# Performance work log

Hardware: AMD Instinct MI355X
Metric: run time of the kernel (lower is better)

## Reference

```python
import jax, jax.numpy as jnp
import numpy as np

B, L = 64, 1024
ENC_DIM, DEC_DIM, ATT_DIM = 512, 512, 512


def setup_inputs() -> dict:
    key = jax.random.key(0)
    ks = jax.random.split(key, 11)
    s_enc = 1.0 / np.sqrt(ENC_DIM)
    s_dec = 1.0 / np.sqrt(DEC_DIM)
    s_att = 1.0 / np.sqrt(ATT_DIM)
    return {
        "encoder_features": jax.random.normal(ks[0], (B, L, ENC_DIM), jnp.float32),
        "decoder_hidden": jax.random.normal(ks[1], (B, DEC_DIM), jnp.float32),
        "coverage": jax.random.uniform(ks[2], (B, L), jnp.float32),
        # nn.Linear params (torch stores weight as [out, in]; we keep [in, out])
        "W_enc": jax.random.uniform(ks[3], (ENC_DIM, ATT_DIM), jnp.float32, -s_enc, s_enc),
        "b_enc": jax.random.uniform(ks[4], (ATT_DIM,), jnp.float32, -s_enc, s_enc),
        "W_dec": jax.random.uniform(ks[5], (DEC_DIM, ATT_DIM), jnp.float32, -s_dec, s_dec),
        "b_dec": jax.random.uniform(ks[6], (ATT_DIM,), jnp.float32, -s_dec, s_dec),
        "W_cov": jax.random.uniform(ks[7], (1, ATT_DIM), jnp.float32, -1.0, 1.0),
        "b_cov": jax.random.uniform(ks[8], (ATT_DIM,), jnp.float32, -1.0, 1.0),
        "W_full": jax.random.uniform(ks[9], (ATT_DIM, 1), jnp.float32, -s_att, s_att),
        "b_full": jax.random.uniform(ks[10], (1,), jnp.float32, -s_att, s_att),
    }


def reference(encoder_features, decoder_hidden, coverage,
              W_enc, b_enc, W_dec, b_dec, W_cov, b_cov, W_full, b_full):
    # att1: [B, L, A]
    att1 = jnp.einsum("ble,ea->bla", encoder_features, W_enc) + b_enc
    # att2: [B, 1, A]
    att2 = (decoder_hidden @ W_dec + b_dec)[:, None, :]
    # att3: coverage[B,L] through Linear(1, A) -> outer product, [B, L, A]
    att3 = coverage[:, :, None] * W_cov[0] + b_cov
    # energy: [B, L]
    energy = (jax.nn.relu(att1 + att2 + att3) @ W_full)[:, :, 0] + b_full[0]
    alpha = jax.nn.softmax(energy, axis=1)  # [B, L]
    new_coverage = coverage + alpha
    attention_weighted_encoding = jnp.einsum("ble,bl->be", encoder_features, alpha)
    return (attention_weighted_encoding, alpha, new_coverage)
```

## Files before the change

### kernel.cpp

```cpp
#include <hip/hip_runtime.h>
#include <cstdint>
#include <cstddef>

#define NB   64
#define NL   1024
#define NA   512
#define NE   512
#define NROWS (NB*NL)

typedef __attribute__((ext_vector_type(8))) short bf16x8;
typedef __attribute__((ext_vector_type(4))) float f32x4;

__device__ __forceinline__ unsigned short f2bf(float x){
    unsigned int u = __float_as_uint(x);
    u += 0x7FFFu + ((u >> 16) & 1u);
    return (unsigned short)(u >> 16);
}

__global__ __launch_bounds__(256) void k_wfrag(const float* __restrict__ Wenc,
                                               unsigned short* __restrict__ wfrag){
    const int g    = blockIdx.x * 256 + threadIdx.x;
    const int lane = g & 63;
    const int n    = (g >> 6) & 31;
    const int ks   = (g >> 11) & 1;
    const int s    = g >> 12;
    const int col  = n * 16 + (lane & 15);
    const int kb   = s * 64 + ks * 32 + (lane >> 4) * 8;
    unsigned int w[4];
    #pragma unroll
    for (int p = 0; p < 4; ++p){
        unsigned short lo = f2bf(Wenc[(size_t)(kb + 2*p    ) * NA + col]);
        unsigned short hi = f2bf(Wenc[(size_t)(kb + 2*p + 1) * NA + col]);
        w[p] = (unsigned int)lo | ((unsigned int)hi << 16);
    }
    ((uint4*)wfrag)[g] = make_uint4(w[0], w[1], w[2], w[3]);
}

__global__ __launch_bounds__(256) void k_base(const float* __restrict__ dh,
                                              const float* __restrict__ Wdec,
                                              const float* __restrict__ bdec,
                                              const float* __restrict__ benc,
                                              const float* __restrict__ bcov,
                                              float* __restrict__ base){
    const int b   = blockIdx.x >> 3;
    const int a0  = (blockIdx.x & 7) * 64;
    const int tid = threadIdx.x;
    const int al  = tid & 63, kg = tid >> 6;
    __shared__ float h[512];
    __shared__ float ps[4][64];
    h[tid]       = dh[b * 512 + tid];
    h[tid + 256] = dh[b * 512 + tid + 256];
    __syncthreads();
    const float* wp = Wdec + (size_t)(kg * 128) * 512 + a0 + al;
    const float* hp = h + kg * 128;
    float s0 = 0.f, s1 = 0.f, s2 = 0.f, s3 = 0.f;
    #pragma unroll
    for (int k = 0; k < 128; k += 4){
        s0 += hp[k + 0] * wp[(size_t)(k + 0) * 512];
        s1 += hp[k + 1] * wp[(size_t)(k + 1) * 512];
        s2 += hp[k + 2] * wp[(size_t)(k + 2) * 512];
        s3 += hp[k + 3] * wp[(size_t)(k + 3) * 512];
    }
    ps[kg][al] = (s0 + s1) + (s2 + s3);
    __syncthreads();
    if (tid < 64){
        const int a = a0 + tid;
        base[b * 512 + a] = ps[0][tid] + ps[1][tid] + ps[2][tid] + ps[3][tid]
                          + bdec[a] + benc[a] + bcov[a];
    }
}

__global__ __launch_bounds__(256, 2) void k_energy(
        const float* __restrict__ enc,
        const float* __restrict__ cov,
        const float* __restrict__ base,
        const unsigned short* __restrict__ wfrag,
        const float* __restrict__ Wcov,
        const float* __restrict__ Wfull,
        float* __restrict__ energy)
{
    __shared__ __align__(16) unsigned char sB[65536];
    __shared__ __align__(16) unsigned char sA[8192];
    __shared__ float sCov[64];
    __shared__ float sEp[4][64];

    const int tid  = threadIdx.x;
    const int wid  = tid >> 6, lane = tid & 63;
    const int r0   = blockIdx.x * 64;
    const int b    = r0 >> 10;

    if (tid < 64) sCov[tid] = cov[r0 + tid];

    f32x4 acc[4][8];
    #pragma unroll
    for (int m = 0; m < 4; ++m)
        #pragma unroll
        for (int n = 0; n < 8; ++n) acc[m][n] = (f32x4){0.f, 0.f, 0.f, 0.f};

    const int rloc = tid >> 2, q = tid & 3;
    const float* arow = enc + (size_t)(r0 + rloc) * NE + q * 16;
    unsigned char* aw = sA + (((q >> 1) * 4 + (rloc >> 4)) * 1024
                              + ((rloc & 15) + 32 * (q & 1)) * 16);
    const unsigned char* bsrc = (const unsigned char*)wfrag + wid * 16384 + lane * 16;
    unsigned char* bdst = sB + wid * 16384;

    for (int s = 0; s < 8; ++s){
        __syncthreads();
        const unsigned char* bs = bsrc + (size_t)s * 65536;
        #pragma unroll
        for (int i = 0; i < 16; ++i){
            __builtin_amdgcn_global_load_lds(
                (__attribute__((address_space(1))) void*)(bs + i * 1024),
                (__attribute__((address_space(3))) void*)(bdst + i * 1024),
                16, 0, 0);
        }
        const float* ap = arow + s * 64;
        float4 v0 = *(const float4*)(ap);
        float4 v1 = *(const float4*)(ap + 4);
        float4 v2 = *(const float4*)(ap + 8);
        float4 v3 = *(const float4*)(ap + 12);
        uint4 f1, f2;
        f1.x = f2bf(v0.x) | ((unsigned)f2bf(v0.y) << 16);
        f1.y = f2bf(v0.z) | ((unsigned)f2bf(v0.w) << 16);
        f1.z = f2bf(v1.x) | ((unsigned)f2bf(v1.y) << 16);
        f1.w = f2bf(v1.z) | ((unsigned)f2bf(v1.w) << 16);
        f2.x = f2bf(v2.x) | ((unsigned)f2bf(v2.y) << 16);
        f2.y = f2bf(v2.z) | ((unsigned)f2bf(v2.w) << 16);
        f2.z = f2bf(v3.x) | ((unsigned)f2bf(v3.y) << 16);
        f2.w = f2bf(v3.z) | ((unsigned)f2bf(v3.w) << 16);
        *(uint4*)(aw)       = f1;
        *(uint4*)(aw + 256) = f2;
        __syncthreads();
        bf16x8 af[2][4];
        #pragma unroll
        for (int ks = 0; ks < 2; ++ks)
            #pragma unroll
            for (int m = 0; m < 4; ++m)
                af[ks][m] = *(const bf16x8*)(sA + (ks*4 + m) * 1024 + lane * 16);
        #pragma unroll
        for (int ks = 0; ks < 2; ++ks){
            #pragma unroll
            for (int n = 0; n < 8; ++n){
                bf16x8 bfr = *(const bf16x8*)(sB + (ks*32 + wid*8 + n) * 1024 + lane * 16);
                #pragma unroll
                for (int m = 0; m < 4; ++m)
                    acc[m][n] = __builtin_amdgcn_mfma_f32_16x16x32_bf16(
                                    af[ks][m], bfr, acc[m][n], 0, 0, 0);
            }
        }
    }

    const int c0 = wid * 128 + (lane & 15);
    float basev[8], wcovv[8], wfullv[8];
    #pragma unroll
    for (int n = 0; n < 8; ++n){
        const int c = c0 + n * 16;
        basev[n]  = base[b * 512 + c];
        wcovv[n]  = Wcov[c];
        wfullv[n] = Wfull[c];
    }
    const int hi = lane >> 4;
    float covr[4][4];
    #pragma unroll
    for (int m = 0; m < 4; ++m)
        #pragma unroll
        for (int r = 0; r < 4; ++r) covr[m][r] = sCov[m*16 + 4*hi + r];
    float epv[4][4] = {};
    #pragma unroll
    for (int m = 0; m < 4; ++m)
        #pragma unroll
        for (int n = 0; n < 8; ++n)
            #pragma unroll
            for (int r = 0; r < 4; ++r){
                float v = acc[m][n][r] + basev[n] + covr[m][r] * wcovv[n];
                v = fmaxf(v, 0.f);
                epv[m][r] += v * wfullv[n];
            }
    #pragma unroll
    for (int m = 0; m < 4; ++m)
        #pragma unroll
        for (int r = 0; r < 4; ++r){
            float v = epv[m][r];
            v += __shfl_xor(v, 1);
            v += __shfl_xor(v, 2);
            v += __shfl_xor(v, 4);
            v += __shfl_xor(v, 8);
            epv[m][r] = v;
        }
    if ((lane & 15) == 0){
        #pragma unroll
        for (int m = 0; m < 4; ++m)
            #pragma unroll
            for (int r = 0; r < 4; ++r)
                sEp[wid][m*16 + 4*hi + r] = epv[m][r];
    }
    __syncthreads();
    if (tid < 64)
        energy[r0 + tid] = sEp[0][tid] + sEp[1][tid] + sEp[2][tid] + sEp[3][tid];
}

#define AWE_OFF   0
#define ALPHA_OFF 32768
#define NCOV_OFF  98304

__global__ __launch_bounds__(256) void k_finish(
        const float* __restrict__ enc, const float* __restrict__ cov,
        const float* __restrict__ energy, float* __restrict__ out)
{
    const int bid = blockIdx.x;
    const int b = bid >> 3, ec = bid & 7;
    const int tid = threadIdx.x;
    __shared__ float sa[1024];
    __shared__ float rb[16];
    __shared__ float ps[4][64];

    float4 ev = ((const float4*)(energy + b * 1024))[tid];
    float mx = fmaxf(fmaxf(ev.x, ev.y), fmaxf(ev.z, ev.w));
    #pragma unroll
    for (int off = 32; off; off >>= 1) mx = fmaxf(mx, __shfl_xor(mx, off));
    if ((tid & 63) == 0) rb[tid >> 6] = mx;
    __syncthreads();
    mx = fmaxf(fmaxf(rb[0], rb[1]), fmaxf(rb[2], rb[3]));
    float e0 = __expf(ev.x - mx), e1 = __expf(ev.y - mx),
          e2 = __expf(ev.z - mx), e3 = __expf(ev.w - mx);
    ((float4*)sa)[tid] = make_float4(e0, e1, e2, e3);
    float sm = e0 + e1 + e2 + e3;
    #pragma unroll
    for (int off = 32; off; off >>= 1) sm += __shfl_xor(sm, off);
    if ((tid & 63) == 0) rb[8 + (tid >> 6)] = sm;
    __syncthreads();
    const float inv = 1.0f / (rb[8] + rb[9] + rb[10] + rb[11]);

    if (ec == 0){
        #pragma unroll
        for (int i = 0; i < 4; ++i){
            const int idx = tid + i * 256;
            const float a = sa[idx] * inv;
            out[ALPHA_OFF + b * 1024 + idx] = a;
            out[NCOV_OFF  + b * 1024 + idx] = cov[b * 1024 + idx] + a;
        }
    }

    const int qt = tid >> 6, cl = tid & 63;
    const float* ep = enc + ((size_t)(b * 1024 + qt * 256)) * 512 + ec * 64 + cl;
    const float* w = sa + qt * 256;
    float a0 = 0.f, a1 = 0.f, a2 = 0.f, a3 = 0.f;
    for (int l = 0; l < 256; l += 4){
        a0 += ep[(size_t)(l + 0) * 512] * w[l + 0];
        a1 += ep[(size_t)(l + 1) * 512] * w[l + 1];
        a2 += ep[(size_t)(l + 2) * 512] * w[l + 2];
        a3 += ep[(size_t)(l + 3) * 512] * w[l + 3];
    }
    ps[qt][cl] = (a0 + a1) + (a2 + a3);
    __syncthreads();
    if (tid < 64)
        out[AWE_OFF + b * 512 + ec * 64 + tid] =
            (ps[0][tid] + ps[1][tid] + ps[2][tid] + ps[3][tid]) * inv;
}

extern "C" void kernel_launch(void* const* d_in, const int* in_sizes, int n_in,
                              void* d_out, int out_size, void* d_ws, size_t ws_size,
                              hipStream_t stream){
    const float* enc   = (const float*)d_in[0];
    const float* dh    = (const float*)d_in[1];
    const float* cov   = (const float*)d_in[2];
    const float* Wenc  = (const float*)d_in[3];
    const float* benc  = (const float*)d_in[4];
    const float* Wdec  = (const float*)d_in[5];
    const float* bdec  = (const float*)d_in[6];
    const float* Wcov  = (const float*)d_in[7];
    const float* bcov  = (const float*)d_in[8];
    const float* Wfull = (const float*)d_in[9];
    float* out = (float*)d_out;

    unsigned short* wfrag = (unsigned short*)d_ws;
    float* base   = (float*)((char*)d_ws + 512 * 1024);
    float* energy = (float*)((char*)d_ws + 640 * 1024);

    k_wfrag <<<128,  256, 0, stream>>>(Wenc, wfrag);
    k_base  <<<512,  256, 0, stream>>>(dh, Wdec, bdec, benc, bcov, base);
    k_energy<<<1024, 256, 0, stream>>>(enc, cov, base, wfrag, Wcov, Wfull, energy);
    k_finish<<<512,  256, 0, stream>>>(enc, cov, energy, out);
}
```

Before: 85.16 us.

## Restructure energy GEMM: 128-row tiles, B fragments in registers, double-buffered A

The energy kernel now processes 128 rows per block with 8 waves, each wave owning 64 output columns. The W_enc fragments are loaded straight from global memory into registers instead of staging the whole 64 KB B tile in LDS. The A tile is double-buffered in LDS so the next k-slice's loads and bf16 conversion overlap the current MFMAs, with one barrier per step. The weight fragment layout is reordered to match. This cuts LDS use and traffic and improves overlap, at the cost of higher register pressure from register-resident B (current and next) with 512-thread blocks.

```diff
diff --git a/kernel.cpp b/kernel.cpp
--- a/kernel.cpp
+++ b/kernel.cpp
@@ -6,7 +6,6 @@
 #define NL   1024
 #define NA   512
 #define NE   512
-#define NROWS (NB*NL)
 
 typedef __attribute__((ext_vector_type(8))) short bf16x8;
 typedef __attribute__((ext_vector_type(4))) float f32x4;
@@ -21,10 +20,11 @@
                                                unsigned short* __restrict__ wfrag){
     const int g    = blockIdx.x * 256 + threadIdx.x;
     const int lane = g & 63;
-    const int n    = (g >> 6) & 31;
-    const int ks   = (g >> 11) & 1;
+    const int n    = (g >> 6) & 3;
+    const int ks   = (g >> 8) & 1;
+    const int cw   = (g >> 9) & 7;
     const int s    = g >> 12;
-    const int col  = n * 16 + (lane & 15);
+    const int col  = cw * 64 + n * 16 + (lane & 15);
     const int kb   = s * 64 + ks * 32 + (lane >> 4) * 8;
     unsigned int w[4];
     #pragma unroll
@@ -70,7 +70,7 @@
     }
 }
 
-__global__ __launch_bounds__(256, 2) void k_energy(
+__global__ __launch_bounds__(512, 2) void k_energy(
         const float* __restrict__ enc,
         const float* __restrict__ cov,
         const float* __restrict__ base,
@@ -79,46 +79,38 @@
         const float* __restrict__ Wfull,
         float* __restrict__ energy)
 {
-    __shared__ __align__(16) unsigned char sB[65536];
-    __shared__ __align__(16) unsigned char sA[8192];
-    __shared__ float sCov[64];
-    __shared__ float sEp[4][64];
+    __shared__ __align__(16) unsigned char sA[2][16384];
+    __shared__ float sEp[8][128];
+    __shared__ float sCov[128];
 
     const int tid  = threadIdx.x;
     const int wid  = tid >> 6, lane = tid & 63;
-    const int r0   = blockIdx.x * 64;
+    const int r0   = blockIdx.x * 128;
     const int b    = r0 >> 10;
 
-    if (tid < 64) sCov[tid] = cov[r0 + tid];
-
-    f32x4 acc[4][8];
-    #pragma unroll
-    for (int m = 0; m < 4; ++m)
-        #pragma unroll
-        for (int n = 0; n < 8; ++n) acc[m][n] = (f32x4){0.f, 0.f, 0.f, 0.f};
+    if (tid < 128) sCov[tid] = cov[r0 + tid];
 
     const int rloc = tid >> 2, q = tid & 3;
     const float* arow = enc + (size_t)(r0 + rloc) * NE + q * 16;
-    unsigned char* aw = sA + (((q >> 1) * 4 + (rloc >> 4)) * 1024
-                              + ((rloc & 15) + 32 * (q & 1)) * 16);
-    const unsigned char* bsrc = (const unsigned char*)wfrag + wid * 16384 + lane * 16;
-    unsigned char* bdst = sB + wid * 16384;
-
-    for (int s = 0; s < 8; ++s){
-        __syncthreads();
-        const unsigned char* bs = bsrc + (size_t)s * 65536;
-        #pragma unroll
-        for (int i = 0; i < 16; ++i){
-            __builtin_amdgcn_global_load_lds(
-                (__attribute__((address_space(1))) void*)(bs + i * 1024),
-                (__attribute__((address_space(3))) void*)(bdst + i * 1024),
-                16, 0, 0);
-        }
-        const float* ap = arow + s * 64;
-        float4 v0 = *(const float4*)(ap);
-        float4 v1 = *(const float4*)(ap + 4);
-        float4 v2 = *(const float4*)(ap + 8);
-        float4 v3 = *(const float4*)(ap + 12);
+    const int awoff = ((q >> 1) * 8 + (rloc >> 4)) * 1024
+                    + ((rloc & 15) + 32 * (q & 1)) * 16;
+
+    const bf16x8* bbase = (const bf16x8*)wfrag + wid * 512 + lane;
+
+    f32x4 acc[8][4];
+    #pragma unroll
+    for (int m = 0; m < 8; ++m)
+        #pragma unroll
+        for (int n = 0; n < 4; ++n) acc[m][n] = (f32x4){0.f, 0.f, 0.f, 0.f};
+
+    bf16x8 bcur[8], bnxt[8];
+    #pragma unroll
+    for (int j = 0; j < 8; ++j) bcur[j] = bbase[j * 64];
+    {
+        float4 v0 = *(const float4*)(arow);
+        float4 v1 = *(const float4*)(arow + 4);
+        float4 v2 = *(const float4*)(arow + 8);
+        float4 v3 = *(const float4*)(arow + 12);
         uint4 f1, f2;
         f1.x = f2bf(v0.x) | ((unsigned)f2bf(v0.y) << 16);
         f1.y = f2bf(v0.z) | ((unsigned)f2bf(v0.w) << 16);
@@ -128,56 +120,84 @@
         f2.y = f2bf(v2.z) | ((unsigned)f2bf(v2.w) << 16);
         f2.z = f2bf(v3.x) | ((unsigned)f2bf(v3.y) << 16);
         f2.w = f2bf(v3.z) | ((unsigned)f2bf(v3.w) << 16);
-        *(uint4*)(aw)       = f1;
-        *(uint4*)(aw + 256) = f2;
+        *(uint4*)(sA[0] + awoff)       = f1;
+        *(uint4*)(sA[0] + awoff + 256) = f2;
+    }
+    __syncthreads();
+
+    #pragma unroll
+    for (int s = 0; s < 8; ++s){
+        const int cb = s & 1;
+        float4 av0, av1, av2, av3;
+        if (s < 7){
+            const float* ap = arow + (s + 1) * 64;
+            av0 = *(const float4*)(ap);
+            av1 = *(const float4*)(ap + 4);
+            av2 = *(const float4*)(ap + 8);
+            av3 = *(const float4*)(ap + 12);
+            const bf16x8* bp = bbase + (s + 1) * 4096;
+            #pragma unroll
+            for (int j = 0; j < 8; ++j) bnxt[j] = bp[j * 64];
+        }
+        #pragma unroll
+        for (int ks = 0; ks < 2; ++ks){
+            bf16x8 af[8];
+            #pragma unroll
+            for (int m = 0; m < 8; ++m)
+                af[m] = *(const bf16x8*)(sA[cb] + (ks * 8 + m) * 1024 + lane * 16);
+            #pragma unroll
+            for (int n = 0; n < 4; ++n)
+                #pragma unroll
+                for (int m = 0; m < 8; ++m)
+                    acc[m][n] = __builtin_amdgcn_mfma_f32_16x16x32_bf16(
+                                    af[m], bcur[ks * 4 + n], acc[m][n], 0, 0, 0);
+        }
+        if (s < 7){
+            uint4 f1, f2;
+            f1.x = f2bf(av0.x) | ((unsigned)f2bf(av0.y) << 16);
+            f1.y = f2bf(av0.z) | ((unsigned)f2bf(av0.w) << 16);
+            f1.z = f2bf(av1.x) | ((unsigned)f2bf(av1.y) << 16);
+            f1.w = f2bf(av1.z) | ((unsigned)f2bf(av1.w) << 16);
+            f2.x = f2bf(av2.x) | ((unsigned)f2bf(av2.y) << 16);
+            f2.y = f2bf(av2.z) | ((unsigned)f2bf(av2.w) << 16);
+            f2.z = f2bf(av3.x) | ((unsigned)f2bf(av3.y) << 16);
+            f2.w = f2bf(av3.z) | ((unsigned)f2bf(av3.w) << 16);
+            *(uint4*)(sA[cb ^ 1] + awoff)       = f1;
+            *(uint4*)(sA[cb ^ 1] + awoff + 256) = f2;
+            #pragma unroll
+            for (int j = 0; j < 8; ++j) bcur[j] = bnxt[j];
+        }
         __syncthreads();
-        bf16x8 af[2][4];
-        #pragma unroll
-        for (int ks = 0; ks < 2; ++ks)
-            #pragma unroll
-            for (int m = 0; m < 4; ++m)
-                af[ks][m] = *(const bf16x8*)(sA + (ks*4 + m) * 1024 + lane * 16);
-        #pragma unroll
-        for (int ks = 0; ks < 2; ++ks){
-            #pragma unroll
-            for (int n = 0; n < 8; ++n){
-                bf16x8 bfr = *(const bf16x8*)(sB + (ks*32 + wid*8 + n) * 1024 + lane * 16);
-                #pragma unroll
-                for (int m = 0; m < 4; ++m)
-                    acc[m][n] = __builtin_amdgcn_mfma_f32_16x16x32_bf16(
-                                    af[ks][m], bfr, acc[m][n], 0, 0, 0);
-            }
-        }
-    }
-
-    const int c0 = wid * 128 + (lane & 15);
-    float basev[8], wcovv[8], wfullv[8];
-    #pragma unroll
-    for (int n = 0; n < 8; ++n){
+    }
+
+    const int c0 = wid * 64 + (lane & 15);
+    float basev[4], wcovv[4], wfullv[4];
+    #pragma unroll
+    for (int n = 0; n < 4; ++n){
         const int c = c0 + n * 16;
         basev[n]  = base[b * 512 + c];
         wcovv[n]  = Wcov[c];
         wfullv[n] = Wfull[c];
     }
     const int hi = lane >> 4;
-    float covr[4][4];
-    #pragma unroll
-    for (int m = 0; m < 4; ++m)
-        #pragma unroll
-        for (int r = 0; r < 4; ++r) covr[m][r] = sCov[m*16 + 4*hi + r];
-    float epv[4][4] = {};
-    #pragma unroll
-    for (int m = 0; m < 4; ++m)
-        #pragma unroll
-        for (int n = 0; n < 8; ++n)
-            #pragma unroll
-            for (int r = 0; r < 4; ++r){
-                float v = acc[m][n][r] + basev[n] + covr[m][r] * wcovv[n];
+    float epv[8][4];
+    #pragma unroll
+    for (int m = 0; m < 8; ++m){
+        #pragma unroll
+        for (int r = 0; r < 4; ++r){
+            const float cv = sCov[m * 16 + 4 * hi + r];
+            float e = 0.f;
+            #pragma unroll
+            for (int n = 0; n < 4; ++n){
+                float v = acc[m][n][r] + basev[n] + cv * wcovv[n];
                 v = fmaxf(v, 0.f);
-                epv[m][r] += v * wfullv[n];
+                e += v * wfullv[n];
             }
-    #pragma unroll
-    for (int m = 0; m < 4; ++m)
+            epv[m][r] = e;
+        }
+    }
+    #pragma unroll
+    for (int m = 0; m < 8; ++m)
         #pragma unroll
         for (int r = 0; r < 4; ++r){
             float v = epv[m][r];
@@ -189,14 +209,15 @@
         }
     if ((lane & 15) == 0){
         #pragma unroll
-        for (int m = 0; m < 4; ++m)
+        for (int m = 0; m < 8; ++m)
             #pragma unroll
             for (int r = 0; r < 4; ++r)
-                sEp[wid][m*16 + 4*hi + r] = epv[m][r];
-    }
-    __syncthreads();
-    if (tid < 64)
-        energy[r0 + tid] = sEp[0][tid] + sEp[1][tid] + sEp[2][tid] + sEp[3][tid];
+                sEp[wid][m * 16 + 4 * hi + r] = epv[m][r];
+    }
+    __syncthreads();
+    if (tid < 128)
+        energy[r0 + tid] = ((sEp[0][tid] + sEp[1][tid]) + (sEp[2][tid] + sEp[3][tid]))
+                         + ((sEp[4][tid] + sEp[5][tid]) + (sEp[6][tid] + sEp[7][tid]));
 }
 
 #define AWE_OFF   0
@@ -279,6 +300,6 @@
 
     k_wfrag <<<128,  256, 0, stream>>>(Wenc, wfrag);
     k_base  <<<512,  256, 0, stream>>>(dh, Wdec, bdec, benc, bcov, base);
-    k_energy<<<1024, 256, 0, stream>>>(enc, cov, base, wfrag, Wcov, Wfull, energy);
+    k_energy<<<512,  512, 0, stream>>>(enc, cov, base, wfrag, Wcov, Wfull, energy);
     k_finish<<<512,  256, 0, stream>>>(enc, cov, energy, out);
 }
```

Result: faster. 78.01 us (-8.4%).
